# Kernel tuning notes

Measured on AMD Instinct MI355X. Metric: run time of the kernel, lower is better.

## Reference

```python
import jax, jax.numpy as jnp
import numpy as np

B, L, H, D = 64, 2048, 1024, 128  # segments, segment length, hidden, input_dim
N = B * L

def swish(z):
    return z * jax.nn.sigmoid(z)

def setup_inputs() -> dict:
    key = jax.random.key(0)
    ks = jax.random.split(key, 10)
    s = 0.02
    x_seeds = jax.random.normal(ks[0], (N, D), dtype=jnp.float32)
    x_nodes = jax.random.normal(ks[1], (N, D), dtype=jnp.float32)
    W_seed = jax.random.normal(ks[2], (H, D), dtype=jnp.float32) * s
    W_node = jax.random.normal(ks[3], (H, D), dtype=jnp.float32) * s
    W1 = jax.random.normal(ks[4], (H, H), dtype=jnp.float32) * s
    b1 = jnp.zeros((H,), dtype=jnp.float32)
    W2 = jax.random.normal(ks[5], (H, H), dtype=jnp.float32) * s
    b2 = jnp.zeros((H,), dtype=jnp.float32)
    w_ns = jax.random.normal(ks[6], (1, H), dtype=jnp.float32) * s   # node_score_layer (zero-init in src; random for nontrivial baseline)
    W_stop = jax.random.normal(ks[7], (2, H), dtype=jnp.float32) * s  # stopping_score_layer
    starts = jnp.arange(B, dtype=jnp.int32) * L
    indptr = jnp.stack([starts, starts + L, starts + L], axis=1)  # (start, end, candidate_end)
    return {"x_seeds": x_seeds, "x_nodes": x_nodes, "W_seed": W_seed, "W_node": W_node,
            "W1": W1, "b1": b1, "W2": W2, "b2": b2, "w_ns": w_ns, "W_stop": W_stop,
            "indptr": indptr}

def reference(x_seeds, x_nodes, W_seed, W_node, W1, b1, W2, b2, w_ns, W_stop, indptr):
    # embeddings + 2-layer Swish MLP
    h = x_seeds @ W_seed.T + x_nodes @ W_node.T            # [N, H]
    h = swish(h @ W1.T + b1)
    h = swish(h @ W2.T + b2)
    node_scores = (h @ w_ns.T)[:, 0]                       # [N]
    # ragged segments (uniform length L) defined by indptr starts
    nb = indptr.shape[0]
    seg_len = h.shape[0] // nb                             # static L
    idx = indptr[:, 0][:, None] + jnp.arange(seg_len)      # [B, L]
    h_seg = h[idx]                                         # [B, L, H]
    stop_node = h_seg.mean(axis=1)                         # [B, H] per-segment mean pool
    node_logits = jax.nn.log_softmax(node_scores[idx], axis=1)          # [B, L]
    stop_logits = jax.nn.log_softmax(stop_node @ W_stop.T, axis=1)      # [B, 2]
    # concat([node_logits + stop0, stop1]) per segment
    return jnp.concatenate([node_logits + stop_logits[:, :1], stop_logits[:, 1:]], axis=1)  # [B, L+1]
```

## Files before the change

### kernel.cpp

```cpp
#include <hip/hip_runtime.h>

typedef float f32x4 __attribute__((ext_vector_type(4)));
typedef __bf16 bf16x8 __attribute__((ext_vector_type(8)));
typedef unsigned short u16x8 __attribute__((ext_vector_type(8)));

#define DEVINL static __device__ __forceinline__

DEVINL unsigned short f2bf(float f) {
    unsigned int u = __builtin_bit_cast(unsigned int, f);
    u += 0x7fffu + ((u >> 16) & 1u);
    return (unsigned short)(u >> 16);
}
DEVINL float bf2f(unsigned short u) {
    unsigned int x = ((unsigned int)u) << 16;
    return __builtin_bit_cast(float, x);
}

#define GLD16(gp, lp)                                                          \
    __builtin_amdgcn_global_load_lds(                                          \
        (const __attribute__((address_space(1))) void*)(gp),                   \
        (__attribute__((address_space(3))) void*)(lp), 16, 0, 0)

__global__ void pack_cat_k(const float* __restrict__ s0, const float* __restrict__ s1,
                           unsigned short* __restrict__ dst, int nchunks) {
    int e = blockIdx.x * 256 + threadIdx.x;
    if (e >= nchunks) return;
    int row = e >> 5, ch = e & 31;
    const float* src = (ch < 16) ? (s0 + (size_t)row * 128 + ch * 8)
                                 : (s1 + (size_t)row * 128 + (ch - 16) * 8);
    float4 a = *(const float4*)src;
    float4 b = *(const float4*)(src + 4);
    u16x8 o;
    o[0] = f2bf(a.x); o[1] = f2bf(a.y); o[2] = f2bf(a.z); o[3] = f2bf(a.w);
    o[4] = f2bf(b.x); o[5] = f2bf(b.y); o[6] = f2bf(b.z); o[7] = f2bf(b.w);
    *(u16x8*)(dst + (size_t)e * 8) = o;
}

__global__ void cvt_k(const float* __restrict__ s, unsigned short* __restrict__ d, int nchunks) {
    int e = blockIdx.x * 256 + threadIdx.x;
    if (e >= nchunks) return;
    float4 a = *(const float4*)(s + (size_t)e * 8);
    float4 b = *(const float4*)(s + (size_t)e * 8 + 4);
    u16x8 o;
    o[0] = f2bf(a.x); o[1] = f2bf(a.y); o[2] = f2bf(a.z); o[3] = f2bf(a.w);
    o[4] = f2bf(b.x); o[5] = f2bf(b.y); o[6] = f2bf(b.z); o[7] = f2bf(b.w);
    *(u16x8*)(d + (size_t)e * 8) = o;
}

template <int EPI>
__global__ void gemm_bt_k(const unsigned short* __restrict__ A,
                          const unsigned short* __restrict__ B,
                          const float* __restrict__ bias,
                          unsigned short* __restrict__ C,
                          int M, int N, int K) {
    __shared__ unsigned short As[128 * 32];
    __shared__ unsigned short Bs[128 * 32];
    const int tid  = threadIdx.x;
    const int lane = tid & 63;
    const int wv   = tid >> 6;
    const int wr   = wv >> 1, wc = wv & 1;
    const int ntn  = N >> 7;

    const int nwg = gridDim.x;
    const int xcd = blockIdx.x & 7, blk = blockIdx.x >> 3;
    const int q = nwg >> 3, rr = nwg & 7;
    const int logical = (xcd < rr ? xcd * (q + 1) : rr * (q + 1) + (xcd - rr) * q) + blk;

    const int im   = logical / ntn, in = logical % ntn;
    const size_t rowA0 = (size_t)im * 128, rowB0 = (size_t)in * 128;

    const int e0 = tid, e1 = tid + 256;
    const int ra0 = e0 >> 2, ca0 = (e0 & 3) * 8;
    const int ra1 = e1 >> 2, ca1 = (e1 & 3) * 8;

    f32x4 acc[4][4] = {};
    const int frow = lane & 15;
    const int kb   = (lane >> 4) * 8;

    for (int k0 = 0; k0 < K; k0 += 32) {
        GLD16(A + (rowA0 + ra0) * K + k0 + ca0, (char*)As + e0 * 16);
        GLD16(A + (rowA0 + ra1) * K + k0 + ca1, (char*)As + e1 * 16);
        GLD16(B + (rowB0 + ra0) * K + k0 + ca0, (char*)Bs + e0 * 16);
        GLD16(B + (rowB0 + ra1) * K + k0 + ca1, (char*)Bs + e1 * 16);
        __syncthreads();

        bf16x8 af[4], bfr[4];
#pragma unroll
        for (int m = 0; m < 4; ++m)
            af[m] = *(const bf16x8*)&As[(wr * 64 + m * 16 + frow) * 32 + kb];
#pragma unroll
        for (int n = 0; n < 4; ++n)
            bfr[n] = *(const bf16x8*)&Bs[(wc * 64 + n * 16 + frow) * 32 + kb];
#pragma unroll
        for (int m = 0; m < 4; ++m)
#pragma unroll
            for (int n = 0; n < 4; ++n)
                acc[m][n] = __builtin_amdgcn_mfma_f32_16x16x32_bf16(af[m], bfr[n], acc[m][n], 0, 0, 0);
        __syncthreads();
    }

    const int r4 = (lane >> 4) * 4;
    const int cc = lane & 15;
#pragma unroll
    for (int n = 0; n < 4; ++n) {
        const int col = (int)rowB0 + wc * 64 + n * 16 + cc;
        const float bv = (EPI == 1) ? bias[col] : 0.0f;
#pragma unroll
        for (int m = 0; m < 4; ++m) {
            const size_t row = rowA0 + wr * 64 + m * 16 + r4;
#pragma unroll
            for (int r = 0; r < 4; ++r) {
                float v = acc[m][n][r] + bv;
                if (EPI == 1) v = v / (1.0f + __expf(-v));
                C[(row + r) * (size_t)N + col] = f2bf(v);
            }
        }
    }
}

DEVINL int swz(int b) { return b ^ (((b >> 9) & 1) << 5); }

template <int BS, int KH, int MH>
DEVINL void phase_mfma(char* smA, char* smB, f32x4 (&acc)[8][4],
                       int wr, int wc, int fr, int kl) {
    bf16x8 aF[4], bF[4];
    char* Ab = smA + BS * 32768 + KH * 16384;
    char* Bb = smB + BS * 32768 + KH * 16384;
#pragma unroll
    for (int x = 0; x < 4; ++x) {
        const int ba = (wr * 128 + MH * 64 + x * 16 + fr) * 64 + kl;
        aF[x] = *(const bf16x8*)(Ab + swz(ba));
        const int bb = (wc * 64 + x * 16 + fr) * 64 + kl;
        bF[x] = *(const bf16x8*)(Bb + swz(bb));
    }
    __builtin_amdgcn_s_barrier();
    __builtin_amdgcn_s_setprio(1);
#pragma unroll
    for (int m2 = 0; m2 < 4; ++m2)
#pragma unroll
        for (int n = 0; n < 4; ++n)
            acc[MH * 4 + m2][n] = __builtin_amdgcn_mfma_f32_16x16x32_bf16(
                aF[m2], bF[n], acc[MH * 4 + m2][n], 0, 0, 0);
    __builtin_amdgcn_s_setprio(0);
    __builtin_amdgcn_s_barrier();
}

#define VMW asm volatile("s_waitcnt vmcnt(4)" ::: "memory")

template <int EPI>
__launch_bounds__(512, 2)
__global__ void gemm256_k(const unsigned short* __restrict__ A,
                          const unsigned short* __restrict__ Bm,
                          const float* __restrict__ bias,
                          unsigned short* __restrict__ C,
                          const float* __restrict__ wns,
                          float* __restrict__ sc,
                          float* __restrict__ pl,
                          int M, int N, int K) {
    extern __shared__ __align__(16) char sm[];
    char* smA = sm;
    char* smB = sm + 65536;
    const int tid  = threadIdx.x;
    const int lane = tid & 63, w = tid >> 6;
    const int wr = w >> 2, wc = w & 3;
    const int fr = lane & 15;
    const int kl = (lane >> 4) * 16;
    const int ntn = N >> 8;

    const int nwg = gridDim.x;
    const int xcd = blockIdx.x & 7, blk = blockIdx.x >> 3;
    const int q = nwg >> 3, rr = nwg & 7;
    const int logical = (xcd < rr ? xcd * (q + 1) : rr * (q + 1) + (xcd - rr) * q) + blk;
    const int im = logical / ntn, in = logical % ntn;
    const size_t rowA0 = (size_t)im * 256, colB0 = (size_t)in * 256;
    const int NT = K >> 6;

    f32x4 acc[8][4] = {};

    auto stage = [&](const unsigned short* G, size_t grow0, int tile, int half, char* dst) {
#pragma unroll
        for (int j = 0; j < 2; ++j) {
            const int c = tid + j * 512;
            const int g = c ^ (((c >> 5) & 1) << 1);
            GLD16(G + (grow0 + (g >> 2)) * K + tile * 64 + half * 32 + (g & 3) * 8,
                  dst + c * 16);
        }
    };

    stage(A, rowA0, 0, 0, smA);
    stage(Bm, colB0, 0, 0, smB);
    stage(A, rowA0, 0, 1, smA + 16384);
    stage(Bm, colB0, 0, 1, smB + 16384);
    stage(A, rowA0, 1, 0, smA + 32768);
    stage(Bm, colB0, 1, 0, smB + 32768);
    VMW;
    __builtin_amdgcn_s_barrier();

    const int NI = NT >> 1;
    for (int i = 0; i < NI; ++i) {
        const int t1 = 2 * i + 1, t2 = 2 * i + 2, t3 = 2 * i + 3;
        stage(A, rowA0, t1, 1, smA + 49152);
        phase_mfma<0, 0, 0>(smA, smB, acc, wr, wc, fr, kl);
        stage(Bm, colB0, t1, 1, smB + 49152);
        phase_mfma<0, 0, 1>(smA, smB, acc, wr, wc, fr, kl);
        if (t2 < NT) stage(A, rowA0, t2, 0, smA);
        phase_mfma<0, 1, 0>(smA, smB, acc, wr, wc, fr, kl);
        if (t2 < NT) stage(Bm, colB0, t2, 0, smB);
        VMW;
        phase_mfma<0, 1, 1>(smA, smB, acc, wr, wc, fr, kl);
        if (t2 < NT) stage(A, rowA0, t2, 1, smA + 16384);
        phase_mfma<1, 0, 0>(smA, smB, acc, wr, wc, fr, kl);
        if (t2 < NT) stage(Bm, colB0, t2, 1, smB + 16384);
        phase_mfma<1, 0, 1>(smA, smB, acc, wr, wc, fr, kl);
        if (t3 < NT) stage(A, rowA0, t3, 0, smA + 32768);
        phase_mfma<1, 1, 0>(smA, smB, acc, wr, wc, fr, kl);
        if (t3 < NT) stage(Bm, colB0, t3, 0, smB + 32768);
        VMW;
        phase_mfma<1, 1, 1>(smA, smB, acc, wr, wc, fr, kl);
    }

    const int r4 = (lane >> 4) * 4;
    const int cc = lane & 15;

    if (EPI == 2) {
#pragma unroll
        for (int n = 0; n < 4; ++n) {
            const float bv = bias[(int)colB0 + wc * 64 + n * 16 + cc];
#pragma unroll
            for (int m = 0; m < 8; ++m)
#pragma unroll
                for (int r = 0; r < 4; ++r) {
                    float v = acc[m][n][r] + bv;
                    acc[m][n][r] = v / (1.0f + __expf(-v));
                }
        }
#pragma unroll
        for (int m = 0; m < 8; ++m)
#pragma unroll
            for (int r = 0; r < 4; ++r) {
                float s = 0.f;
#pragma unroll
                for (int n = 0; n < 4; ++n)
                    s += acc[m][n][r] * wns[(int)colB0 + wc * 64 + n * 16 + cc];
#pragma unroll
                for (int o = 1; o < 16; o <<= 1) s += __shfl_xor(s, o);
                if (cc == 0)
                    atomicAdd(&sc[rowA0 + wr * 128 + m * 16 + r4 + r], s);
            }
        const int seg = (int)(rowA0 >> 11);
#pragma unroll
        for (int n = 0; n < 4; ++n) {
            float p = 0.f;
#pragma unroll
            for (int m = 0; m < 8; ++m)
#pragma unroll
                for (int r = 0; r < 4; ++r) p += acc[m][n][r];
            p += __shfl_xor(p, 16);
            p += __shfl_xor(p, 32);
            if ((lane >> 4) == 0)
                atomicAdd(&pl[seg * 1024 + (int)colB0 + wc * 64 + n * 16 + cc],
                          p * (1.0f / 2048.0f));
        }
        return;
    }

#pragma unroll
    for (int n = 0; n < 4; ++n) {
        const int col = (int)colB0 + wc * 64 + n * 16 + cc;
        const float bv = bias[col];
#pragma unroll
        for (int m = 0; m < 8; ++m) {
            const size_t row = rowA0 + wr * 128 + m * 16 + r4;
#pragma unroll
            for (int r = 0; r < 4; ++r) {
                float v = acc[m][n][r] + bv;
                v = v / (1.0f + __expf(-v));
                C[(row + r) * (size_t)N + col] = f2bf(v);
            }
        }
    }
}

__global__ void stop_k(const float* __restrict__ pool, const float* __restrict__ Wstop,
                       float* __restrict__ stp, float* __restrict__ out) {
    const int b = blockIdx.x, t = threadIdx.x;
    float a0 = 0.f, a1 = 0.f;
#pragma unroll
    for (int j = 0; j < 4; ++j) {
        const int hcol = t + j * 256;
        const float pv = pool[b * 1024 + hcol];
        a0 += pv * Wstop[hcol];
        a1 += pv * Wstop[1024 + hcol];
    }
    const int lane = t & 63, wv = t >> 6;
#pragma unroll
    for (int off = 32; off; off >>= 1) { a0 += __shfl_down(a0, off); a1 += __shfl_down(a1, off); }
    __shared__ float r0[4], r1[4];
    if (lane == 0) { r0[wv] = a0; r1[wv] = a1; }
    __syncthreads();
    if (t == 0) {
        const float s0 = r0[0] + r0[1] + r0[2] + r0[3];
        const float s1 = r1[0] + r1[1] + r1[2] + r1[3];
        const float m  = fmaxf(s0, s1);
        const float lse = m + __logf(__expf(s0 - m) + __expf(s1 - m));
        stp[b * 2] = s0 - lse;
        out[(size_t)b * 2049 + 2048] = s1 - lse;
    }
}

__global__ void node_k(const float* __restrict__ sc, const float* __restrict__ stp,
                       float* __restrict__ out) {
    const int b = blockIdx.x, t = threadIdx.x;
    const float* s = sc + (size_t)b * 2048;
    float v[8];
    float mx = -3.4e38f;
#pragma unroll
    for (int j = 0; j < 8; ++j) { v[j] = s[t + j * 256]; mx = fmaxf(mx, v[j]); }
    const int lane = t & 63, wv = t >> 6;
    __shared__ float red[4];
#pragma unroll
    for (int off = 32; off; off >>= 1) mx = fmaxf(mx, __shfl_down(mx, off));
    if (lane == 0) red[wv] = mx;
    __syncthreads();
    mx = fmaxf(fmaxf(red[0], red[1]), fmaxf(red[2], red[3]));
    float se = 0.f;
#pragma unroll
    for (int j = 0; j < 8; ++j) se += __expf(v[j] - mx);
    __syncthreads();
#pragma unroll
    for (int off = 32; off; off >>= 1) se += __shfl_down(se, off);
    if (lane == 0) red[wv] = se;
    __syncthreads();
    se = red[0] + red[1] + red[2] + red[3];
    const float base = stp[b * 2] - mx - __logf(se);
#pragma unroll
    for (int j = 0; j < 8; ++j) out[(size_t)b * 2049 + t + j * 256] = v[j] + base;
}

extern "C" void kernel_launch(void* const* d_in, const int* in_sizes, int n_in,
                              void* d_out, int out_size, void* d_ws, size_t ws_size,
                              hipStream_t stream) {
    (void)in_sizes; (void)n_in; (void)out_size;
    const float* x_seeds = (const float*)d_in[0];
    const float* x_nodes = (const float*)d_in[1];
    const float* W_seed  = (const float*)d_in[2];
    const float* W_node  = (const float*)d_in[3];
    const float* W1      = (const float*)d_in[4];
    const float* b1      = (const float*)d_in[5];
    const float* W2      = (const float*)d_in[6];
    const float* b2      = (const float*)d_in[7];
    const float* w_ns    = (const float*)d_in[8];
    const float* W_stop  = (const float*)d_in[9];
    float* out = (float*)d_out;

    const int N = 131072, H = 1024, B = 64;

    {
        auto f1 = gemm256_k<1>; auto f2 = gemm256_k<2>;
        hipFuncSetAttribute((const void*)f1, hipFuncAttributeMaxDynamicSharedMemorySize, 131072);
        hipFuncSetAttribute((const void*)f2, hipFuncAttributeMaxDynamicSharedMemorySize, 131072);
    }

    char* ws = (char*)d_ws;
    size_t off = 0;
    auto alloc = [&](size_t bytes) {
        char* p = ws + off;
        off += (bytes + 255) & ~(size_t)255;
        return p;
    };
    unsigned short* wcat = (unsigned short*)alloc((size_t)H * 256 * 2);
    unsigned short* W1b  = (unsigned short*)alloc((size_t)H * H * 2);
    unsigned short* W2b  = (unsigned short*)alloc((size_t)H * H * 2);
    float* scores = (float*)alloc((size_t)N * 4);
    float* pool   = (float*)alloc((size_t)B * H * 4);
    float* stp    = (float*)alloc((size_t)B * 2 * 4);

    const size_t per_row = 256 * 2 + 1024 * 2 + 1024 * 2;
    size_t avail = (ws_size > off + (1u << 20)) ? (ws_size - off - (1u << 20)) : 0;
    long long mc_ll = (long long)(avail / per_row) / 2048 * 2048;
    int Mc = (int)(mc_ll < 2048 ? 2048 : (mc_ll > 65536 ? 65536 : mc_ll));

    unsigned short* xcat_c = (unsigned short*)alloc((size_t)Mc * 256 * 2);
    unsigned short* h0_c   = (unsigned short*)alloc((size_t)Mc * H * 2);
    unsigned short* h1_c   = (unsigned short*)alloc((size_t)Mc * H * 2);

    hipMemsetAsync(pool, 0, (size_t)B * H * 4, stream);
    hipMemsetAsync(scores, 0, (size_t)N * 4, stream);

    pack_cat_k<<<(H * 32) / 256, 256, 0, stream>>>(W_seed, W_node, wcat, H * 32);
    cvt_k<<<(H * H / 8) / 256, 256, 0, stream>>>(W1, W1b, H * H / 8);
    cvt_k<<<(H * H / 8) / 256, 256, 0, stream>>>(W2, W2b, H * H / 8);

    for (int base = 0; base < N; base += Mc) {
        const int m = (N - base < Mc) ? (N - base) : Mc;
        pack_cat_k<<<(m * 32) / 256, 256, 0, stream>>>(
            x_seeds + (size_t)base * 128, x_nodes + (size_t)base * 128, xcat_c, m * 32);
        const int grid128 = (m / 128) * (H / 128);
        gemm_bt_k<0><<<grid128, 256, 0, stream>>>(xcat_c, wcat, nullptr, h0_c, m, H, 256);
        const int grid256 = (m / 256) * (H / 256);
        gemm256_k<1><<<grid256, 512, 131072, stream>>>(h0_c, W1b, b1, h1_c,
                                                       nullptr, nullptr, nullptr, m, H, H);
        gemm256_k<2><<<grid256, 512, 131072, stream>>>(h1_c, W2b, b2, nullptr,
                                                       w_ns, scores + base,
                                                       pool + (size_t)(base / 2048) * H, m, H, H);
    }

    stop_k<<<B, 256, 0, stream>>>(pool, W_stop, stp, out);
    node_k<<<B, 256, 0, stream>>>(scores, stp, out);
}
```

Before: 1.062 ms.

## Restructure 256x256 GEMM mainloop into quadrant phases with full-K-tile LDS layout

Reworks the bf16 GEMM main loop so each phase computes one (M-half, N-half) quadrant over the full 64-wide K tile. Staging is rebuilt around 128-byte rows with a 3-bit XOR swizzle, and global-to-LDS loads are interleaved per phase with vmcnt(8) waits plus explicit tail phases. Warp-to-output mapping changes to interleaved 64x32 sub-tiles, and the epilogues are updated to match. Launch bounds drop to 1 block per CU, which gives more registers but lowers occupancy.

```diff
diff --git a/kernel.cpp b/kernel.cpp
--- a/kernel.cpp
+++ b/kernel.cpp
@@ -118,37 +118,49 @@
     }
 }
 
-DEVINL int swz(int b) { return b ^ (((b >> 9) & 1) << 5); }
-
-template <int BS, int KH, int MH>
-DEVINL void phase_mfma(char* smA, char* smB, f32x4 (&acc)[8][4],
-                       int wr, int wc, int fr, int kl) {
-    bf16x8 aF[4], bF[4];
-    char* Ab = smA + BS * 32768 + KH * 16384;
-    char* Bb = smB + BS * 32768 + KH * 16384;
-#pragma unroll
-    for (int x = 0; x < 4; ++x) {
-        const int ba = (wr * 128 + MH * 64 + x * 16 + fr) * 64 + kl;
-        aF[x] = *(const bf16x8*)(Ab + swz(ba));
-        const int bb = (wc * 64 + x * 16 + fr) * 64 + kl;
-        bF[x] = *(const bf16x8*)(Bb + swz(bb));
-    }
+DEVINL int swz16(int b) { return b ^ (((b >> 7) & 7) << 4); }
+
+template <int W>
+DEVINL void vmw() {
+    if constexpr (W == 8) asm volatile("s_waitcnt vmcnt(8)" ::: "memory");
+    else if constexpr (W == 4) asm volatile("s_waitcnt vmcnt(4)" ::: "memory");
+    else if constexpr (W == 0) asm volatile("s_waitcnt vmcnt(0)" ::: "memory");
+}
+
+template <int MH, int NH, int W, typename F>
+DEVINL void qphase(char* smA, char* smB, int p, f32x4 (&acc)[8][4],
+                   int wr, int wc, int fr, int kg, F&& stg) {
+    char* Ab = smA + p * 32768 + MH * 16384;
+    char* Bb = smB + p * 32768 + NH * 16384;
+    bf16x8 aF[4][2], bF[2][2];
+#pragma unroll
+    for (int m2 = 0; m2 < 4; ++m2)
+#pragma unroll
+        for (int kk = 0; kk < 2; ++kk)
+            aF[m2][kk] = *(const bf16x8*)(Ab + swz16((wr * 64 + m2 * 16 + fr) * 128 + kk * 64 + kg));
+#pragma unroll
+    for (int n2 = 0; n2 < 2; ++n2)
+#pragma unroll
+        for (int kk = 0; kk < 2; ++kk)
+            bF[n2][kk] = *(const bf16x8*)(Bb + swz16((wc * 32 + n2 * 16 + fr) * 128 + kk * 64 + kg));
+    stg();
+    vmw<W>();
     __builtin_amdgcn_s_barrier();
     __builtin_amdgcn_s_setprio(1);
 #pragma unroll
-    for (int m2 = 0; m2 < 4; ++m2)
-#pragma unroll
-        for (int n = 0; n < 4; ++n)
-            acc[MH * 4 + m2][n] = __builtin_amdgcn_mfma_f32_16x16x32_bf16(
-                aF[m2], bF[n], acc[MH * 4 + m2][n], 0, 0, 0);
+    for (int kk = 0; kk < 2; ++kk)
+#pragma unroll
+        for (int m2 = 0; m2 < 4; ++m2)
+#pragma unroll
+            for (int n2 = 0; n2 < 2; ++n2)
+                acc[MH * 4 + m2][NH * 2 + n2] = __builtin_amdgcn_mfma_f32_16x16x32_bf16(
+                    aF[m2][kk], bF[n2][kk], acc[MH * 4 + m2][NH * 2 + n2], 0, 0, 0);
     __builtin_amdgcn_s_setprio(0);
     __builtin_amdgcn_s_barrier();
 }
 
-#define VMW asm volatile("s_waitcnt vmcnt(4)" ::: "memory")
-
 template <int EPI>
-__launch_bounds__(512, 2)
+__launch_bounds__(512, 1)
 __global__ void gemm256_k(const unsigned short* __restrict__ A,
                           const unsigned short* __restrict__ Bm,
                           const float* __restrict__ bias,
@@ -164,7 +176,7 @@
     const int lane = tid & 63, w = tid >> 6;
     const int wr = w >> 2, wc = w & 3;
     const int fr = lane & 15;
-    const int kl = (lane >> 4) * 16;
+    const int kg = (lane >> 4) * 16;
     const int ntn = N >> 8;
 
     const int nwg = gridDim.x;
@@ -177,46 +189,52 @@
 
     f32x4 acc[8][4] = {};
 
-    auto stage = [&](const unsigned short* G, size_t grow0, int tile, int half, char* dst) {
+    auto stageA = [&](int tile, int half, int par) {
 #pragma unroll
         for (int j = 0; j < 2; ++j) {
             const int c = tid + j * 512;
-            const int g = c ^ (((c >> 5) & 1) << 1);
-            GLD16(G + (grow0 + (g >> 2)) * K + tile * 64 + half * 32 + (g & 3) * 8,
-                  dst + c * 16);
+            const int gc = (c & 7) ^ ((c >> 3) & 7);
+            GLD16(A + (rowA0 + half * 128 + (c >> 3)) * K + tile * 64 + gc * 8,
+                  smA + par * 32768 + half * 16384 + c * 16);
         }
     };
-
-    stage(A, rowA0, 0, 0, smA);
-    stage(Bm, colB0, 0, 0, smB);
-    stage(A, rowA0, 0, 1, smA + 16384);
-    stage(Bm, colB0, 0, 1, smB + 16384);
-    stage(A, rowA0, 1, 0, smA + 32768);
-    stage(Bm, colB0, 1, 0, smB + 32768);
-    VMW;
+    auto stageB = [&](int tile, int half, int par) {
+#pragma unroll
+        for (int j = 0; j < 2; ++j) {
+            const int c = tid + j * 512;
+            const int gc = (c & 7) ^ ((c >> 3) & 7);
+            GLD16(Bm + (colB0 + half * 128 + (c >> 3)) * K + tile * 64 + gc * 8,
+                  smB + par * 32768 + half * 16384 + c * 16);
+        }
+    };
+    auto nop = [] {};
+
+    stageA(0, 0, 0); stageB(0, 0, 0);
+    stageB(0, 1, 0); stageA(0, 1, 0);
+    stageA(1, 0, 1); stageB(1, 0, 1);
+    vmw<8>();
     __builtin_amdgcn_s_barrier();
 
-    const int NI = NT >> 1;
-    for (int i = 0; i < NI; ++i) {
-        const int t1 = 2 * i + 1, t2 = 2 * i + 2, t3 = 2 * i + 3;
-        stage(A, rowA0, t1, 1, smA + 49152);
-        phase_mfma<0, 0, 0>(smA, smB, acc, wr, wc, fr, kl);
-        stage(Bm, colB0, t1, 1, smB + 49152);
-        phase_mfma<0, 0, 1>(smA, smB, acc, wr, wc, fr, kl);
-        if (t2 < NT) stage(A, rowA0, t2, 0, smA);
-        phase_mfma<0, 1, 0>(smA, smB, acc, wr, wc, fr, kl);
-        if (t2 < NT) stage(Bm, colB0, t2, 0, smB);
-        VMW;
-        phase_mfma<0, 1, 1>(smA, smB, acc, wr, wc, fr, kl);
-        if (t2 < NT) stage(A, rowA0, t2, 1, smA + 16384);
-        phase_mfma<1, 0, 0>(smA, smB, acc, wr, wc, fr, kl);
-        if (t2 < NT) stage(Bm, colB0, t2, 1, smB + 16384);
-        phase_mfma<1, 0, 1>(smA, smB, acc, wr, wc, fr, kl);
-        if (t3 < NT) stage(A, rowA0, t3, 0, smA + 32768);
-        phase_mfma<1, 1, 0>(smA, smB, acc, wr, wc, fr, kl);
-        if (t3 < NT) stage(Bm, colB0, t3, 0, smB + 32768);
-        VMW;
-        phase_mfma<1, 1, 1>(smA, smB, acc, wr, wc, fr, kl);
+    for (int t = 0; t + 2 < NT; ++t) {
+        const int p = t & 1;
+        qphase<0, 0, 8>(smA, smB, p, acc, wr, wc, fr, kg, [&] { stageB(t + 1, 1, p ^ 1); });
+        qphase<0, 1, 8>(smA, smB, p, acc, wr, wc, fr, kg, [&] { stageA(t + 1, 1, p ^ 1); });
+        qphase<1, 0, 8>(smA, smB, p, acc, wr, wc, fr, kg, [&] { stageA(t + 2, 0, p); });
+        qphase<1, 1, 8>(smA, smB, p, acc, wr, wc, fr, kg, [&] { stageB(t + 2, 0, p); });
+    }
+    {
+        const int t = NT - 2, p = t & 1;
+        qphase<0, 0, 8>(smA, smB, p, acc, wr, wc, fr, kg, [&] { stageB(t + 1, 1, p ^ 1); });
+        qphase<0, 1, 8>(smA, smB, p, acc, wr, wc, fr, kg, [&] { stageA(t + 1, 1, p ^ 1); });
+        qphase<1, 0, 4>(smA, smB, p, acc, wr, wc, fr, kg, nop);
+        qphase<1, 1, 0>(smA, smB, p, acc, wr, wc, fr, kg, nop);
+    }
+    {
+        const int p = (NT - 1) & 1;
+        qphase<0, 0, -1>(smA, smB, p, acc, wr, wc, fr, kg, nop);
+        qphase<0, 1, -1>(smA, smB, p, acc, wr, wc, fr, kg, nop);
+        qphase<1, 0, -1>(smA, smB, p, acc, wr, wc, fr, kg, nop);
+        qphase<1, 1, -1>(smA, smB, p, acc, wr, wc, fr, kg, nop);
     }
 
     const int r4 = (lane >> 4) * 4;
@@ -225,7 +243,7 @@
     if (EPI == 2) {
 #pragma unroll
         for (int n = 0; n < 4; ++n) {
-            const float bv = bias[(int)colB0 + wc * 64 + n * 16 + cc];
+            const float bv = bias[(int)colB0 + (n >> 1) * 128 + wc * 32 + (n & 1) * 16 + cc];
 #pragma unroll
             for (int m = 0; m < 8; ++m)
 #pragma unroll
@@ -241,36 +259,36 @@
                 float s = 0.f;
 #pragma unroll
                 for (int n = 0; n < 4; ++n)
-                    s += acc[m][n][r] * wns[(int)colB0 + wc * 64 + n * 16 + cc];
+                    s += acc[m][n][r] * wns[(int)colB0 + (n >> 1) * 128 + wc * 32 + (n & 1) * 16 + cc];
 #pragma unroll
                 for (int o = 1; o < 16; o <<= 1) s += __shfl_xor(s, o);
                 if (cc == 0)
-                    atomicAdd(&sc[rowA0 + wr * 128 + m * 16 + r4 + r], s);
+                    atomicAdd(&sc[rowA0 + (m >> 2) * 128 + wr * 64 + (m & 3) * 16 + r4 + r], s);
             }
         const int seg = (int)(rowA0 >> 11);
 #pragma unroll
         for (int n = 0; n < 4; ++n) {
-            float p = 0.f;
+            float p2 = 0.f;
 #pragma unroll
             for (int m = 0; m < 8; ++m)
 #pragma unroll
-                for (int r = 0; r < 4; ++r) p += acc[m][n][r];
-            p += __shfl_xor(p, 16);
-            p += __shfl_xor(p, 32);
+                for (int r = 0; r < 4; ++r) p2 += acc[m][n][r];
+            p2 += __shfl_xor(p2, 16);
+            p2 += __shfl_xor(p2, 32);
             if ((lane >> 4) == 0)
-                atomicAdd(&pl[seg * 1024 + (int)colB0 + wc * 64 + n * 16 + cc],
-                          p * (1.0f / 2048.0f));
+                atomicAdd(&pl[seg * 1024 + (int)colB0 + (n >> 1) * 128 + wc * 32 + (n & 1) * 16 + cc],
+                          p2 * (1.0f / 2048.0f));
         }
         return;
     }
 
 #pragma unroll
     for (int n = 0; n < 4; ++n) {
-        const int col = (int)colB0 + wc * 64 + n * 16 + cc;
+        const int col = (int)colB0 + (n >> 1) * 128 + wc * 32 + (n & 1) * 16 + cc;
         const float bv = bias[col];
 #pragma unroll
         for (int m = 0; m < 8; ++m) {
-            const size_t row = rowA0 + wr * 128 + m * 16 + r4;
+            const size_t row = rowA0 + (m >> 2) * 128 + wr * 64 + (m & 3) * 16 + r4;
 #pragma unroll
             for (int r = 0; r < 4; ++r) {
                 float v = acc[m][n][r] + bv;
```

Result: slower. 1.094 ms (+3.0%).
